# Optimization experiments

Measured on AMD Instinct MI355X. Metric: run time of the kernel, lower is better.

## Reference

```python
import jax, jax.numpy as jnp
import numpy as np

B, C, H, W = 4, 16, 320, 640


def _propagate_front(x, g):
    """Linear propagation along leading axis.
    x, g: [L, ...]. out[0] = x[0]; out[i] = x[i]*(1-g[i]) + g[i]*out[i-1].
    """
    def step(prev, xg):
        xr, gr = xg
        out = xr * (1.0 - gr) + gr * prev
        return out, out
    _, ys = jax.lax.scan(step, x[0], (x[1:], g[1:]))
    return jnp.concatenate([x[:1], ys], axis=0)


def _propagate(x, g, axis, reverse):
    xm = jnp.moveaxis(x, axis, 0)
    gm = jnp.moveaxis(g, axis, 0)
    if reverse:
        xm = xm[::-1]
        gm = gm[::-1]
    ym = _propagate_front(xm, gm)
    if reverse:
        ym = ym[::-1]
    return jnp.moveaxis(ym, 0, axis)


def setup_inputs() -> dict:
    key = jax.random.key(0)
    ks = jax.random.split(key, 5)
    shape = (B, C, H, W)
    return {
        "input": jax.random.normal(ks[0], shape, dtype=jnp.float32),
        "g0": jax.random.uniform(ks[1], shape, dtype=jnp.float32),
        "g1": jax.random.uniform(ks[2], shape, dtype=jnp.float32),
        "g2": jax.random.uniform(ks[3], shape, dtype=jnp.float32),
        "g3": jax.random.uniform(ks[4], shape, dtype=jnp.float32),
    }


def reference(input, g0, g1, g2, g3):
    # 4-directional gated recurrent grid propagation, fused by elementwise max.
    r_down = _propagate(input, g0, axis=2, reverse=False)   # top -> bottom over H
    r_up = _propagate(input, g1, axis=2, reverse=True)      # bottom -> top over H
    r_right = _propagate(input, g2, axis=3, reverse=False)  # left -> right over W
    r_left = _propagate(input, g3, axis=3, reverse=True)    # right -> left over W
    return jnp.maximum(jnp.maximum(jnp.maximum(r_down, r_up), r_right), r_left)
```

## Files before the change

### kernel.cpp

```cpp
#include <hip/hip_runtime.h>

constexpr int Bn = 4;
constexpr int Cn = 16;
constexpr int Hn = 320;
constexpr int Wn = 640;
constexpr int NCOL = Bn * Cn * Wn;
constexpr int NROW = Bn * Cn * Hn;

constexpr int HS = 10;
constexpr int NS = 32;
constexpr int TC = 32;
constexpr int CPB = TC * 4;
constexpr int GPW = Wn / CPB;
constexpr int W4 = Wn / 4;

#define REP10(M) M(0) M(1) M(2) M(3) M(4) M(5) M(6) M(7) M(8) M(9)
#define REP10R(M) M(9) M(8) M(7) M(6) M(5) M(4) M(3) M(2) M(1) M(0)

#define SCAN4(gv, xv, yy, pp)                                         \
  yy.x = fmaf(gv.x, yy.x - xv.x, xv.x); pp.x *= gv.x;                 \
  yy.y = fmaf(gv.y, yy.y - xv.y, xv.y); pp.y *= gv.y;                 \
  yy.z = fmaf(gv.z, yy.z - xv.z, xv.z); pp.z *= gv.z;                 \
  yy.w = fmaf(gv.w, yy.w - xv.w, xv.w); pp.w *= gv.w;

__global__ __launch_bounds__(1024)
__attribute__((amdgpu_waves_per_eu(4, 4))) void vert_both(
    const float* __restrict__ x, const float* __restrict__ g0,
    const float* __restrict__ g1, float* __restrict__ vm) {
  __shared__ float4 As[NS][TC], Bs[NS][TC];
  const int grp = blockIdx.x;
  const int bc = grp / GPW;
  const int q0 = (grp % GPW) * TC;
  const int s = threadIdx.x >> 5;
  const int tc = threadIdx.x & 31;
  const int base = bc * (Hn * W4) + (s * HS) * W4 + q0 + tc;
  const float4* x4 = (const float4*)x;
  const float4* g04 = (const float4*)g0;
  const float4* g14 = (const float4*)g1;
  float4* vm4 = (float4*)vm;

#define DECLD(i) float4 rd##i, pd##i;
  REP10(DECLD)
#undef DECLD

  {
    int off = base;
    float4 yy = make_float4(0.f, 0.f, 0.f, 0.f);
    float4 pp = make_float4(1.f, 1.f, 1.f, 1.f);
#define DSTEP(i)                                                      \
    {                                                                 \
      float4 xv = x4[off];                                            \
      float4 gv = g04[off];                                           \
      if (s == 0 && i == 0) gv = make_float4(0.f, 0.f, 0.f, 0.f);     \
      SCAN4(gv, xv, yy, pp)                                           \
      rd##i = yy;                                                     \
      pd##i = pp;                                                     \
      off += W4;                                                      \
    }
    REP10(DSTEP)
#undef DSTEP
    As[s][tc] = yy;
    Bs[s][tc] = pp;
  }
  __syncthreads();
  if (threadIdx.x < 32) {
    const int t = threadIdx.x;
    float4 c = make_float4(0.f, 0.f, 0.f, 0.f);
#pragma unroll
    for (int ss = 0; ss < NS; ++ss) {
      float4 a = As[ss][t], b = Bs[ss][t];
      As[ss][t] = c;
      c.x = fmaf(b.x, c.x, a.x);
      c.y = fmaf(b.y, c.y, a.y);
      c.z = fmaf(b.z, c.z, a.z);
      c.w = fmaf(b.w, c.w, a.w);
    }
  }
  __syncthreads();

  {
    const float4 cd = As[s][tc];
#define FIXD(i)                                                       \
    rd##i.x = fmaf(pd##i.x, cd.x, rd##i.x);                           \
    rd##i.y = fmaf(pd##i.y, cd.y, rd##i.y);                           \
    rd##i.z = fmaf(pd##i.z, cd.z, rd##i.z);                           \
    rd##i.w = fmaf(pd##i.w, cd.w, rd##i.w);
    REP10(FIXD)
#undef FIXD
  }

#define DECLU(i) float4 yu##i, pu##i;
  REP10(DECLU)
#undef DECLU
  {
    int off = base + (HS - 1) * W4;
    float4 yy = make_float4(0.f, 0.f, 0.f, 0.f);
    float4 pp = make_float4(1.f, 1.f, 1.f, 1.f);
#define USTEP(i)                                                      \
    {                                                                 \
      float4 xv = x4[off];                                            \
      float4 gv = g14[off];                                           \
      if (s == NS - 1 && i == HS - 1) gv = make_float4(0.f, 0.f, 0.f, 0.f); \
      SCAN4(gv, xv, yy, pp)                                           \
      yu##i = yy;                                                     \
      pu##i = pp;                                                     \
      off -= W4;                                                      \
    }
    REP10R(USTEP)
#undef USTEP
    As[s][tc] = yy;
    Bs[s][tc] = pp;
  }
  __syncthreads();
  if (threadIdx.x < 32) {
    const int t = threadIdx.x;
    float4 c = make_float4(0.f, 0.f, 0.f, 0.f);
#pragma unroll
    for (int ss = NS - 1; ss >= 0; --ss) {
      float4 a = As[ss][t], b = Bs[ss][t];
      As[ss][t] = c;
      c.x = fmaf(b.x, c.x, a.x);
      c.y = fmaf(b.y, c.y, a.y);
      c.z = fmaf(b.z, c.z, a.z);
      c.w = fmaf(b.w, c.w, a.w);
    }
  }
  __syncthreads();

  {
    const float4 cu = As[s][tc];
    int off = base;
#define FSTEP(i)                                                      \
    {                                                                 \
      float4 o;                                                       \
      o.x = fmaxf(rd##i.x, fmaf(pu##i.x, cu.x, yu##i.x));             \
      o.y = fmaxf(rd##i.y, fmaf(pu##i.y, cu.y, yu##i.y));             \
      o.z = fmaxf(rd##i.z, fmaf(pu##i.z, cu.z, yu##i.z));             \
      o.w = fmaxf(rd##i.w, fmaf(pu##i.w, cu.w, yu##i.w));             \
      vm4[off] = o;                                                   \
      off += W4;                                                      \
    }
    REP10(FSTEP)
#undef FSTEP
  }
}

constexpr int WSEG = 10;

__global__ __launch_bounds__(256) void horiz_final(
    const float* __restrict__ x, const float* __restrict__ g2,
    const float* __restrict__ g3, const float* __restrict__ vm,
    float* __restrict__ out) {
  __shared__ float xs[4 * Wn], rrs[4 * Wn], rls[4 * Wn];
  const int tid = threadIdx.x, wv = tid >> 6, l = tid & 63;
  const size_t rowbase = (size_t)blockIdx.x * 4 * Wn;

  const float4* xg = (const float4*)(x + rowbase);
  const float4* g2g = (const float4*)(g2 + rowbase);
  const float4* g3g = (const float4*)(g3 + rowbase);
  const float4* vm4 = (const float4*)(vm + rowbase);
  float4* xsv = (float4*)xs;
  float4* rrv = (float4*)rrs;
  float4* rlv = (float4*)rls;

  const int i0 = tid, i1 = tid + 256, i2 = tid + 512;
  float4 v0, v1, v2;
  xsv[i0] = xg[i0]; rrv[i0] = g2g[i0]; rlv[i0] = g3g[i0]; v0 = vm4[i0];
  xsv[i1] = xg[i1]; rrv[i1] = g2g[i1]; rlv[i1] = g3g[i1]; v1 = vm4[i1];
  if (i2 < Wn) { xsv[i2] = xg[i2]; rrv[i2] = g2g[i2]; rlv[i2] = g3g[i2]; v2 = vm4[i2]; }
  __syncthreads();

  const int rb = wv * Wn + l * WSEG;
  float xl[WSEG], gl[WSEG], yl[WSEG], pl[WSEG];
#pragma unroll
  for (int i = 0; i < WSEG; ++i) { xl[i] = xs[rb + i]; gl[i] = rrs[rb + i]; }

  {
    float y = 0.0f, p = 1.0f;
#pragma unroll
    for (int i = 0; i < WSEG; ++i) {
      float bb = (l == 0 && i == 0) ? 0.0f : gl[i];
      y = fmaf(bb, y - xl[i], xl[i]);
      p *= bb;
      yl[i] = y; pl[i] = p;
    }
    float A = y, B = p;
#pragma unroll
    for (int off = 1; off < 64; off <<= 1) {
      float Au = __shfl_up(A, off);
      float Bu = __shfl_up(B, off);
      if (l >= off) { A = fmaf(B, Au, A); B *= Bu; }
    }
    float c = __shfl_up(A, 1);
    if (l == 0) c = 0.0f;
#pragma unroll
    for (int i = 0; i < WSEG; ++i) rrs[rb + i] = fmaf(pl[i], c, yl[i]);
  }

#pragma unroll
  for (int i = 0; i < WSEG; ++i) gl[i] = rls[rb + i];
  {
    float y = 0.0f, p = 1.0f;
#pragma unroll
    for (int i = WSEG - 1; i >= 0; --i) {
      float bb = (l == 63 && i == WSEG - 1) ? 0.0f : gl[i];
      y = fmaf(bb, y - xl[i], xl[i]);
      p *= bb;
      yl[i] = y; pl[i] = p;
    }
    float A = y, B = p;
#pragma unroll
    for (int off = 1; off < 64; off <<= 1) {
      float Ad = __shfl_down(A, off);
      float Bd = __shfl_down(B, off);
      if (l + off < 64) { A = fmaf(B, Ad, A); B *= Bd; }
    }
    float c = __shfl_down(A, 1);
    if (l == 63) c = 0.0f;
#pragma unroll
    for (int i = 0; i < WSEG; ++i) rls[rb + i] = fmaf(pl[i], c, yl[i]);
  }
  __syncthreads();

  float4* o4 = (float4*)(out + rowbase);
  {
    float4 a = rrv[i0], b = rlv[i0];
    float4 o;
    o.x = fmaxf(fmaxf(a.x, b.x), v0.x);
    o.y = fmaxf(fmaxf(a.y, b.y), v0.y);
    o.z = fmaxf(fmaxf(a.z, b.z), v0.z);
    o.w = fmaxf(fmaxf(a.w, b.w), v0.w);
    o4[i0] = o;
  }
  {
    float4 a = rrv[i1], b = rlv[i1];
    float4 o;
    o.x = fmaxf(fmaxf(a.x, b.x), v1.x);
    o.y = fmaxf(fmaxf(a.y, b.y), v1.y);
    o.z = fmaxf(fmaxf(a.z, b.z), v1.z);
    o.w = fmaxf(fmaxf(a.w, b.w), v1.w);
    o4[i1] = o;
  }
  if (i2 < Wn) {
    float4 a = rrv[i2], b = rlv[i2];
    float4 o;
    o.x = fmaxf(fmaxf(a.x, b.x), v2.x);
    o.y = fmaxf(fmaxf(a.y, b.y), v2.y);
    o.z = fmaxf(fmaxf(a.z, b.z), v2.z);
    o.w = fmaxf(fmaxf(a.w, b.w), v2.w);
    o4[i2] = o;
  }
}

extern "C" void kernel_launch(void* const* d_in, const int* in_sizes, int n_in,
                              void* d_out, int out_size, void* d_ws,
                              size_t ws_size, hipStream_t stream) {
  const float* x = (const float*)d_in[0];
  const float* g0 = (const float*)d_in[1];
  const float* g1 = (const float*)d_in[2];
  const float* g2 = (const float*)d_in[3];
  const float* g3 = (const float*)d_in[4];
  float* out = (float*)d_out;

  vert_both<<<NCOL / CPB, 1024, 0, stream>>>(x, g0, g1, out);
  horiz_final<<<NROW / 4, 256, 0, stream>>>(x, g2, g3, out, out);
}
```

Before: 321.5 us.

## Narrow vertical scan to float2 and spill down results through global memory

```diff
diff --git a/kernel.cpp b/kernel.cpp
--- a/kernel.cpp
+++ b/kernel.cpp
@@ -10,52 +10,45 @@
 constexpr int HS = 10;
 constexpr int NS = 32;
 constexpr int TC = 32;
-constexpr int CPB = TC * 4;
+constexpr int CPB = TC * 2;
 constexpr int GPW = Wn / CPB;
-constexpr int W4 = Wn / 4;
+constexpr int W2 = Wn / 2;
 
 #define REP10(M) M(0) M(1) M(2) M(3) M(4) M(5) M(6) M(7) M(8) M(9)
 #define REP10R(M) M(9) M(8) M(7) M(6) M(5) M(4) M(3) M(2) M(1) M(0)
 
-#define SCAN4(gv, xv, yy, pp)                                         \
-  yy.x = fmaf(gv.x, yy.x - xv.x, xv.x); pp.x *= gv.x;                 \
-  yy.y = fmaf(gv.y, yy.y - xv.y, xv.y); pp.y *= gv.y;                 \
-  yy.z = fmaf(gv.z, yy.z - xv.z, xv.z); pp.z *= gv.z;                 \
-  yy.w = fmaf(gv.w, yy.w - xv.w, xv.w); pp.w *= gv.w;
-
-__global__ __launch_bounds__(1024)
-__attribute__((amdgpu_waves_per_eu(4, 4))) void vert_both(
+__global__ __launch_bounds__(1024) void vert_both(
     const float* __restrict__ x, const float* __restrict__ g0,
     const float* __restrict__ g1, float* __restrict__ vm) {
-  __shared__ float4 As[NS][TC], Bs[NS][TC];
+  __shared__ float2 As[NS][TC], Bs[NS][TC];
   const int grp = blockIdx.x;
   const int bc = grp / GPW;
   const int q0 = (grp % GPW) * TC;
   const int s = threadIdx.x >> 5;
   const int tc = threadIdx.x & 31;
-  const int base = bc * (Hn * W4) + (s * HS) * W4 + q0 + tc;
-  const float4* x4 = (const float4*)x;
-  const float4* g04 = (const float4*)g0;
-  const float4* g14 = (const float4*)g1;
-  float4* vm4 = (float4*)vm;
-
-#define DECLD(i) float4 rd##i, pd##i;
+  const int base = bc * (Hn * W2) + (s * HS) * W2 + q0 + tc;
+  const float2* x2 = (const float2*)x;
+  const float2* g02 = (const float2*)g0;
+  const float2* g12 = (const float2*)g1;
+  float2* vm2 = (float2*)vm;
+
+#define DECLD(i) float2 rd##i, pd##i;
   REP10(DECLD)
 #undef DECLD
-
   {
     int off = base;
-    float4 yy = make_float4(0.f, 0.f, 0.f, 0.f);
-    float4 pp = make_float4(1.f, 1.f, 1.f, 1.f);
+    float2 yy = make_float2(0.f, 0.f);
+    float2 pp = make_float2(1.f, 1.f);
 #define DSTEP(i)                                                      \
     {                                                                 \
-      float4 xv = x4[off];                                            \
-      float4 gv = g04[off];                                           \
-      if (s == 0 && i == 0) gv = make_float4(0.f, 0.f, 0.f, 0.f);     \
-      SCAN4(gv, xv, yy, pp)                                           \
+      float2 xv = x2[off];                                            \
+      float2 gv = g02[off];                                           \
+      if (s == 0 && i == 0) gv = make_float2(0.f, 0.f);               \
+      yy.x = fmaf(gv.x, yy.x - xv.x, xv.x); pp.x *= gv.x;             \
+      yy.y = fmaf(gv.y, yy.y - xv.y, xv.y); pp.y *= gv.y;             \
       rd##i = yy;                                                     \
       pd##i = pp;                                                     \
-      off += W4;                                                      \
+      off += W2;                                                      \
     }
     REP10(DSTEP)
 #undef DSTEP
@@ -65,46 +58,49 @@
   __syncthreads();
   if (threadIdx.x < 32) {
     const int t = threadIdx.x;
-    float4 c = make_float4(0.f, 0.f, 0.f, 0.f);
+    float2 c = make_float2(0.f, 0.f);
 #pragma unroll
     for (int ss = 0; ss < NS; ++ss) {
-      float4 a = As[ss][t], b = Bs[ss][t];
+      float2 a = As[ss][t], b = Bs[ss][t];
       As[ss][t] = c;
       c.x = fmaf(b.x, c.x, a.x);
       c.y = fmaf(b.y, c.y, a.y);
-      c.z = fmaf(b.z, c.z, a.z);
-      c.w = fmaf(b.w, c.w, a.w);
-    }
-  }
-  __syncthreads();
-
-  {
-    const float4 cd = As[s][tc];
-#define FIXD(i)                                                       \
-    rd##i.x = fmaf(pd##i.x, cd.x, rd##i.x);                           \
-    rd##i.y = fmaf(pd##i.y, cd.y, rd##i.y);                           \
-    rd##i.z = fmaf(pd##i.z, cd.z, rd##i.z);                           \
-    rd##i.w = fmaf(pd##i.w, cd.w, rd##i.w);
-    REP10(FIXD)
-#undef FIXD
-  }
-
-#define DECLU(i) float4 yu##i, pu##i;
+    }
+  }
+  __syncthreads();
+
+  {
+    const float2 cd = As[s][tc];
+    int off = base;
+#define FSTORE(i)                                                     \
+    {                                                                 \
+      float2 d;                                                       \
+      d.x = fmaf(pd##i.x, cd.x, rd##i.x);                             \
+      d.y = fmaf(pd##i.y, cd.y, rd##i.y);                             \
+      vm2[off] = d;                                                   \
+      off += W2;                                                      \
+    }
+    REP10(FSTORE)
+#undef FSTORE
+  }
+
+#define DECLU(i) float2 yu##i, pu##i;
   REP10(DECLU)
 #undef DECLU
   {
-    int off = base + (HS - 1) * W4;
-    float4 yy = make_float4(0.f, 0.f, 0.f, 0.f);
-    float4 pp = make_float4(1.f, 1.f, 1.f, 1.f);
+    int off = base + (HS - 1) * W2;
+    float2 yy = make_float2(0.f, 0.f);
+    float2 pp = make_float2(1.f, 1.f);
 #define USTEP(i)                                                      \
     {                                                                 \
-      float4 xv = x4[off];                                            \
-      float4 gv = g14[off];                                           \
-      if (s == NS - 1 && i == HS - 1) gv = make_float4(0.f, 0.f, 0.f, 0.f); \
-      SCAN4(gv, xv, yy, pp)                                           \
+      float2 xv = x2[off];                                            \
+      float2 gv = g12[off];                                           \
+      if (s == NS - 1 && i == HS - 1) gv = make_float2(0.f, 0.f);     \
+      yy.x = fmaf(gv.x, yy.x - xv.x, xv.x); pp.x *= gv.x;             \
+      yy.y = fmaf(gv.y, yy.y - xv.y, xv.y); pp.y *= gv.y;             \
       yu##i = yy;                                                     \
       pu##i = pp;                                                     \
-      off -= W4;                                                      \
+      off -= W2;                                                      \
     }
     REP10R(USTEP)
 #undef USTEP
@@ -114,34 +110,31 @@
   __syncthreads();
   if (threadIdx.x < 32) {
     const int t = threadIdx.x;
-    float4 c = make_float4(0.f, 0.f, 0.f, 0.f);
+    float2 c = make_float2(0.f, 0.f);
 #pragma unroll
     for (int ss = NS - 1; ss >= 0; --ss) {
-      float4 a = As[ss][t], b = Bs[ss][t];
+      float2 a = As[ss][t], b = Bs[ss][t];
       As[ss][t] = c;
       c.x = fmaf(b.x, c.x, a.x);
       c.y = fmaf(b.y, c.y, a.y);
-      c.z = fmaf(b.z, c.z, a.z);
-      c.w = fmaf(b.w, c.w, a.w);
-    }
-  }
-  __syncthreads();
-
-  {
-    const float4 cu = As[s][tc];
+    }
+  }
+  __syncthreads();
+
+  {
+    const float2 cu = As[s][tc];
     int off = base;
-#define FSTEP(i)                                                      \
-    {                                                                 \
-      float4 o;                                                       \
-      o.x = fmaxf(rd##i.x, fmaf(pu##i.x, cu.x, yu##i.x));             \
-      o.y = fmaxf(rd##i.y, fmaf(pu##i.y, cu.y, yu##i.y));             \
-      o.z = fmaxf(rd##i.z, fmaf(pu##i.z, cu.z, yu##i.z));             \
-      o.w = fmaxf(rd##i.w, fmaf(pu##i.w, cu.w, yu##i.w));             \
-      vm4[off] = o;                                                   \
-      off += W4;                                                      \
-    }
-    REP10(FSTEP)
-#undef FSTEP
+#define RSTEP(i)                                                      \
+    {                                                                 \
+      float2 dv = vm2[off];                                           \
+      float2 o;                                                       \
+      o.x = fmaxf(dv.x, fmaf(pu##i.x, cu.x, yu##i.x));                \
+      o.y = fmaxf(dv.y, fmaf(pu##i.y, cu.y, yu##i.y));                \
+      vm2[off] = o;                                                   \
+      off += W2;                                                      \
+    }
+    REP10(RSTEP)
+#undef RSTEP
   }
 }
 
```

New measurement: 273.2 us. 15.0% less time.
